# Performance work log

Measured on AMD Instinct MI355X. Metric: run time of the kernel, lower is better.

Reference implementation:

```python
import jax, jax.numpy as jnp
import numpy as np

N_EXPERTS = 8
TOP_K = 2


def setup_inputs() -> dict:
    key = jax.random.key(0)
    ks = jax.random.split(key, 5)
    B, T, D, E, H = 4, 2048, 1024, N_EXPERTS, 2730  # H = int(2*D*4/3)
    x = jax.random.normal(ks[0], (B, T, D), dtype=jnp.float32)
    gate_w = jax.random.normal(ks[1], (E, D), dtype=jnp.float32) * 0.02
    w1 = jax.random.normal(ks[2], (E, H, D), dtype=jnp.float32) * 0.02
    w3 = jax.random.normal(ks[3], (E, H, D), dtype=jnp.float32) * 0.02
    w2 = jax.random.normal(ks[4], (E, D, H), dtype=jnp.float32) * 0.02
    return {"x": x, "gate_w": gate_w, "w1": w1, "w3": w3, "w2": w2}


def reference(x, gate_w, w1, w3, w2):
    B, T, D = x.shape
    E = gate_w.shape[0]
    x_flat = x.reshape(-1, D)  # [N, D], N = B*T
    N = x_flat.shape[0]

    # Router: top-k over softmax probabilities, renormalized over selected experts
    logits = x_flat @ gate_w.T                      # [N, E]
    probs = jax.nn.softmax(logits, axis=-1)         # [N, E]
    top_v, top_i = jax.lax.top_k(probs, TOP_K)      # [N, K]
    top_v = top_v / jnp.sum(top_v, axis=-1, keepdims=True)

    # Dense combine weights [N, E]: weight of expert e for each token (0 if not selected).
    # top_k indices are distinct per token, so scatter-add equals scatter-set here.
    combine = jnp.zeros((N, E), dtype=x.dtype).at[
        jnp.arange(N)[:, None], top_i
    ].add(top_v)

    # Weighted combine of SwiGLU experts (loop over small fixed expert count).
    out = jnp.zeros_like(x_flat)
    for e in range(E):
        gate = jax.nn.silu(x_flat @ w1[e].T)        # [N, H]
        up = x_flat @ w3[e].T                       # [N, H]
        y = (gate * up) @ w2[e].T                   # [N, D]
        out = out + combine[:, e:e + 1] * y

    aux_loss = jnp.asarray(0.0, dtype=x.dtype)  # use_aux_loss=False / eval mode
    return out.reshape(B, T, D), aux_loss
```

## Files before the change

### kernel.cpp

```cpp
#include <hip/hip_runtime.h>
#include <hip/hip_bf16.h>

#define N_TOK 8192
#define D_DIM 1024
#define E_NUM 8
#define H_DIM 2730
#define HP    2816
#define NP    5632
#define NROWS (N_TOK*2)
#define MAXTILES 136
#define MAXT256  72

typedef __bf16 bf16;
typedef __bf16 bf16x8 __attribute__((ext_vector_type(8)));
typedef __bf16 bf16x4 __attribute__((ext_vector_type(4)));
typedef float  f32x4  __attribute__((ext_vector_type(4)));

__device__ __forceinline__ void gload_lds16(const bf16* g, bf16* l) {
  __builtin_amdgcn_global_load_lds((const __attribute__((address_space(1))) void*)g,
                                   (__attribute__((address_space(3))) void*)l, 16, 0, 0);
}
#define VMCNT(n) asm volatile("s_waitcnt vmcnt(" #n ")" ::: "memory")
#define BAR() __builtin_amdgcn_s_barrier()

__global__ void conv13_kernel(const float* __restrict__ w1, const float* __restrict__ w3,
                              bf16* __restrict__ Bp) {
  int i = blockIdx.x * blockDim.x + threadIdx.x;
  if (i >= E_NUM * NP * 128) return;
  int c8 = i & 127;
  int r  = (i >> 7) % NP;
  int e  = i / (NP * 128);
  int hc = ((r >> 5) << 4) + (r & 15);
  bf16x8 o;
  if (hc < H_DIM) {
    const float* s = (((r >> 4) & 1) ? w3 : w1) + ((long)e * H_DIM + hc) * D_DIM + c8 * 8;
    float4 a0 = ((const float4*)s)[0], a1 = ((const float4*)s)[1];
    o[0]=(bf16)a0.x; o[1]=(bf16)a0.y; o[2]=(bf16)a0.z; o[3]=(bf16)a0.w;
    o[4]=(bf16)a1.x; o[5]=(bf16)a1.y; o[6]=(bf16)a1.z; o[7]=(bf16)a1.w;
  } else {
    #pragma unroll
    for (int j = 0; j < 8; j++) o[j] = (bf16)0.f;
  }
  ((bf16x8*)Bp)[i] = o;
}

__global__ void conv_w2_kernel(const float* __restrict__ src, bf16* __restrict__ dst) {
  int i = blockIdx.x * blockDim.x + threadIdx.x;
  if (i >= E_NUM * D_DIM * (HP / 8)) return;
  int c8 = i % (HP / 8);
  int row = i / (HP / 8);
  int c = c8 * 8;
  const float* s = src + (long)row * H_DIM + c;
  bf16x8 o;
  #pragma unroll
  for (int j = 0; j < 8; j++) o[j] = (c + j < H_DIM) ? (bf16)s[j] : (bf16)0.f;
  ((bf16x8*)dst)[i] = o;
}

__global__ void router_kernel(const float* __restrict__ x, const float* __restrict__ gw,
                              int* __restrict__ topi, float* __restrict__ topw,
                              int* __restrict__ counts) {
  int t = blockIdx.x * (blockDim.x >> 6) + (threadIdx.x >> 6);
  int lane = threadIdx.x & 63;
  if (t >= N_TOK) return;
  const float* xr = x + (long)t * D_DIM;
  float acc[E_NUM];
  #pragma unroll
  for (int e = 0; e < E_NUM; e++) acc[e] = 0.f;
  for (int j = 0; j < D_DIM / 64; j++) {
    float xv = xr[j * 64 + lane];
    #pragma unroll
    for (int e = 0; e < E_NUM; e++) acc[e] += xv * gw[e * D_DIM + j * 64 + lane];
  }
  #pragma unroll
  for (int e = 0; e < E_NUM; e++) {
    float v = acc[e];
    #pragma unroll
    for (int s = 32; s > 0; s >>= 1) v += __shfl_xor(v, s, 64);
    acc[e] = v;
  }
  if (lane == 0) {
    int b0 = -1, b1 = -1; float v0 = -1e30f, v1 = -1e30f;
    #pragma unroll
    for (int e = 0; e < E_NUM; e++) {
      float v = acc[e];
      if (v > v0) { v1 = v0; b1 = b0; v0 = v; b0 = e; }
      else if (v > v1) { v1 = v; b1 = e; }
    }
    float w0 = 1.f / (1.f + expf(v1 - v0));
    topi[t * 2] = b0; topi[t * 2 + 1] = b1;
    topw[t * 2] = w0; topw[t * 2 + 1] = 1.f - w0;
    atomicAdd(&counts[b0], 1); atomicAdd(&counts[b1], 1);
  }
}

__global__ void tiles_kernel(const int* __restrict__ counts, int* __restrict__ offs,
                             int* __restrict__ tlist, int* __restrict__ tlist2) {
  if (threadIdx.x == 0) {
    int s = 0, idx = 0, idx2 = 0;
    for (int e = 0; e < E_NUM; e++) {
      offs[e] = s;
      int ne = counts[e];
      s += ne;
      int nt = (ne + 127) >> 7;
      for (int t = 0; t < nt; t++) tlist[idx++] = (e << 8) | t;
      int nt2 = (ne + 255) >> 8;
      for (int t = 0; t < nt2; t++) tlist2[idx2++] = (e << 8) | t;
    }
    offs[E_NUM] = s;
    for (; idx < MAXTILES; idx++) tlist[idx] = -1;
    for (; idx2 < MAXT256; idx2++) tlist2[idx2] = -1;
  }
}

__global__ void scatter_kernel(const int* __restrict__ topi, const float* __restrict__ topw,
                               const int* __restrict__ offs, int* __restrict__ cursor,
                               int* __restrict__ rowmap, float* __restrict__ roww,
                               int* __restrict__ rowoftok) {
  int i = blockIdx.x * blockDim.x + threadIdx.x;
  if (i >= NROWS) return;
  int e = topi[i];
  int pos = atomicAdd(&cursor[e], 1);
  int row = offs[e] + pos;
  rowmap[row] = i >> 1;
  roww[row] = topw[i];
  rowoftok[i] = row;
}

__global__ void gather_kernel(const float* __restrict__ x, const int* __restrict__ rowmap,
                              bf16* __restrict__ Xg) {
  int r = blockIdx.x * (blockDim.x >> 6) + (threadIdx.x >> 6);
  int lane = threadIdx.x & 63;
  if (r >= NROWS) return;
  int t = rowmap[r];
  const float4* src = (const float4*)(x + (long)t * D_DIM);
  bf16x4* dst = (bf16x4*)(Xg + (long)r * D_DIM);
  #pragma unroll
  for (int j = 0; j < 4; j++) {
    float4 v = src[j * 64 + lane];
    bf16x4 o; o[0]=(bf16)v.x; o[1]=(bf16)v.y; o[2]=(bf16)v.z; o[3]=(bf16)v.w;
    dst[j * 64 + lane] = o;
  }
}

__global__ void combine_kernel(const bf16* __restrict__ y, const int* __restrict__ rowoftok,
                               const float* __restrict__ topw, float* __restrict__ out) {
  int t = blockIdx.x * (blockDim.x >> 6) + (threadIdx.x >> 6);
  int lane = threadIdx.x & 63;
  if (t >= N_TOK) return;
  int r0 = rowoftok[t * 2], r1 = rowoftok[t * 2 + 1];
  float w0 = topw[t * 2], w1 = topw[t * 2 + 1];
  const bf16x8* y0 = (const bf16x8*)(y + (long)r0 * D_DIM);
  const bf16x8* y1 = (const bf16x8*)(y + (long)r1 * D_DIM);
  float* o = out + (long)t * D_DIM;
  #pragma unroll
  for (int j = 0; j < 2; j++) {
    bf16x8 a = y0[j * 64 + lane], b = y1[j * 64 + lane];
    float4 v0, v1;
    v0.x = w0*(float)a[0] + w1*(float)b[0]; v0.y = w0*(float)a[1] + w1*(float)b[1];
    v0.z = w0*(float)a[2] + w1*(float)b[2]; v0.w = w0*(float)a[3] + w1*(float)b[3];
    v1.x = w0*(float)a[4] + w1*(float)b[4]; v1.y = w0*(float)a[5] + w1*(float)b[5];
    v1.z = w0*(float)a[6] + w1*(float)b[6]; v1.w = w0*(float)a[7] + w1*(float)b[7];
    float4* op = (float4*)(o + (j * 64 + lane) * 8);
    op[0] = v0; op[1] = v1;
  }
}

#define G1_READ_A(MH, OB) do { \
    _Pragma("unroll") for (int m_ = 0; m_ < 4; m_++) \
    _Pragma("unroll") for (int ks_ = 0; ks_ < 2; ks_++) \
      aF[m_][ks_] = *(const bf16x8*)&smem[(OB) + ((MH)*128 + wr*64 + m_*16 + fr)*64 + ((ks_*4 + hi) ^ fr7)*8]; \
  } while (0)
#define G1_READ_B(NH, OB) do { \
    _Pragma("unroll") for (int n_ = 0; n_ < 2; n_++) \
    _Pragma("unroll") for (int ks_ = 0; ks_ < 2; ks_++) \
      bF[n_][ks_] = *(const bf16x8*)&smem[(OB) + 16384 + ((NH)*128 + wc*32 + n_*16 + fr)*64 + ((ks_*4 + hi) ^ fr7)*8]; \
  } while (0)
#define G1_MFMA(MH, NH) do { \
    __builtin_amdgcn_s_setprio(1); \
    _Pragma("unroll") for (int m_ = 0; m_ < 4; m_++) \
    _Pragma("unroll") for (int n_ = 0; n_ < 2; n_++) \
    _Pragma("unroll") for (int ks_ = 0; ks_ < 2; ks_++) \
      acc[MH][NH][m_][n_] = __builtin_amdgcn_mfma_f32_16x16x32_bf16(aF[m_][ks_], bF[n_][ks_], acc[MH][NH][m_][n_], 0, 0, 0); \
    __builtin_amdgcn_s_setprio(0); \
  } while (0)
#define G1_STAGE_A(NB, HM, KT) do { \
    _Pragma("unroll") for (int L_ = 0; L_ < 2; L_++) \
      gload_lds16(aP[HM][L_] + (KT)*64, smem + (NB)*32768 + ((HM)*128 + wv*16 + L_*8)*64); \
  } while (0)
#define G1_STAGE_B(NB, HM, KT) do { \
    _Pragma("unroll") for (int L_ = 0; L_ < 2; L_++) \
      gload_lds16(bP[HM][L_] + (KT)*64, smem + (NB)*32768 + 16384 + ((HM)*128 + wv*16 + L_*8)*64); \
  } while (0)

__global__ __launch_bounds__(512, 2) void gemm1_kernel(
    const bf16* __restrict__ Xg, const bf16* __restrict__ Bp,
    const int* __restrict__ counts, const int* __restrict__ offs,
    const int* __restrict__ tlist2, bf16* __restrict__ h) {
  int te = tlist2[blockIdx.x];
  if (te < 0) return;
  int e = te >> 8, tm = te & 255;
  int ne = counts[e];
  int row_base = offs[e];
  int n0 = blockIdx.y * 256;

  __shared__ bf16 smem[2 * 32768];
  int tid = threadIdx.x, wv = tid >> 6, lane = tid & 63;
  int wr = wv >> 2, wc = wv & 3;
  int fr = lane & 15, hi = lane >> 4, fr7 = lane & 7;
  int l8 = lane >> 3;
  int sx = ((lane & 7) ^ (l8 & 7)) * 8;

  f32x4 acc[2][2][4][2];
  #pragma unroll
  for (int a = 0; a < 2; a++)
    #pragma unroll
    for (int b = 0; b < 2; b++)
      #pragma unroll
      for (int m = 0; m < 4; m++)
        #pragma unroll
        for (int n = 0; n < 2; n++) acc[a][b][m][n] = (f32x4)0.f;

  const bf16* Bpe = Bp + (long)e * NP * D_DIM;
  const bf16* aP[2][2];
  const bf16* bP[2][2];
  #pragma unroll
  for (int hm = 0; hm < 2; hm++)
    #pragma unroll
    for (int L = 0; L < 2; L++) {
      int rt = tm * 256 + hm * 128 + wv * 16 + L * 8 + l8;
      aP[hm][L] = Xg + (long)(row_base + min(rt, ne - 1)) * D_DIM + sx;
      int rb = n0 + hm * 128 + wv * 16 + L * 8 + l8;
      bP[hm][L] = Bpe + (long)rb * D_DIM + sx;
    }

  bf16x8 aF[4][2], bF[2][2];

  G1_STAGE_B(0, 0, 0); G1_STAGE_A(0, 0, 0); G1_STAGE_A(0, 1, 0); G1_STAGE_B(0, 1, 0);
  VMCNT(4); BAR();

  for (int t = 0; t < 15; t++) {
    int ob = (t & 1) << 15;
    int nb = (t + 1) & 1;
    G1_READ_A(0, ob); G1_READ_B(0, ob);
    G1_STAGE_B(nb, 0, t + 1);
    VMCNT(4); BAR(); G1_MFMA(0, 0); BAR();
    G1_READ_A(1, ob);
    G1_STAGE_A(nb, 0, t + 1);
    VMCNT(4); BAR(); G1_MFMA(1, 0); BAR();
    G1_READ_B(1, ob);
    G1_STAGE_A(nb, 1, t + 1);
    BAR(); G1_MFMA(1, 1); BAR();
    G1_READ_A(0, ob);
    G1_STAGE_B(nb, 1, t + 1);
    VMCNT(4); BAR(); G1_MFMA(0, 1); BAR();
  }
  {
    const int ob = 32768;
    G1_READ_A(0, ob); G1_READ_B(0, ob);
    VMCNT(2); BAR(); G1_MFMA(0, 0); BAR();
    G1_READ_A(1, ob);
    VMCNT(0); BAR(); G1_MFMA(1, 0); BAR();
    G1_READ_B(1, ob);
    BAR(); G1_MFMA(1, 1); BAR();
    G1_READ_A(0, ob);
    G1_MFMA(0, 1);
  }

  int crow4 = hi * 4, ccol = fr;
  #pragma unroll
  for (int mh = 0; mh < 2; mh++)
    #pragma unroll
    for (int m = 0; m < 4; m++)
      #pragma unroll
      for (int j = 0; j < 4; j++) {
        int rloc = tm * 256 + mh * 128 + wr * 64 + m * 16 + crow4 + j;
        if (rloc < ne) {
          long hrow = (long)(row_base + rloc) * HP;
          #pragma unroll
          for (int nh = 0; nh < 2; nh++) {
            int hc0 = (n0 + nh * 128 + wc * 32) >> 1;
            float g = acc[mh][nh][m][0][j], u = acc[mh][nh][m][1][j];
            h[hrow + hc0 + ccol] = (bf16)((g / (1.f + __expf(-g))) * u);
          }
        }
      }
}

#define G2_STAGE(OFF, K0) do { \
    _Pragma("unroll") for (int i_ = 0; i_ < 2; i_++) \
      gload_lds16(aptr[i_] + (K0), &smem2[(OFF) + (i_ * 4 + w) * 512]); \
    _Pragma("unroll") for (int j_ = 0; j_ < 4; j_++) \
      gload_lds16(bptr[j_] + (K0), &smem2[(OFF) + 4096 + (j_ * 4 + w) * 512]); \
  } while (0)
#define G2_COMPUTE(OFF) do { \
    bf16x8 af[4], bfr[8]; \
    _Pragma("unroll") for (int m_ = 0; m_ < 4; m_++) af[m_] = *(const bf16x8*)&smem2[(OFF) + (wr * 64 + m_ * 16 + fr) * 32 + qp]; \
    _Pragma("unroll") for (int n_ = 0; n_ < 8; n_++) bfr[n_] = *(const bf16x8*)&smem2[(OFF) + 4096 + (wc * 128 + n_ * 16 + fr) * 32 + qp]; \
    __builtin_amdgcn_s_setprio(1); \
    _Pragma("unroll") for (int m_ = 0; m_ < 4; m_++) \
    _Pragma("unroll") for (int n_ = 0; n_ < 8; n_++) \
      acc[m_][n_] = __builtin_amdgcn_mfma_f32_16x16x32_bf16(af[m_], bfr[n_], acc[m_][n_], 0, 0, 0); \
    __builtin_amdgcn_s_setprio(0); \
  } while (0)

__global__ __launch_bounds__(256, 2) void gemm2_kernel(
    const bf16* __restrict__ h, const bf16* __restrict__ w2b,
    const int* __restrict__ counts, const int* __restrict__ offs,
    const int* __restrict__ tlist, bf16* __restrict__ y) {
  int te = tlist[blockIdx.x];
  if (te < 0) return;
  int e = te >> 8, tm = te & 255;
  int ne = counts[e];
  int row_base = offs[e];
  int n0 = blockIdx.y * 256;

  __shared__ bf16 smem2[3 * 12288];
  int tid = threadIdx.x, w = tid >> 6, lane = tid & 63;
  int wr = w >> 1, wc = w & 1;
  int seg_c = (((lane & 3) ^ ((lane >> 3) & 3))) * 8;
  int fr = lane & 15;
  int qp = (((lane >> 4) ^ ((fr >> 1) & 3))) * 8;

  f32x4 acc[4][8];
  #pragma unroll
  for (int m = 0; m < 4; m++)
    #pragma unroll
    for (int n = 0; n < 8; n++) acc[m][n] = (f32x4)0.f;

  const bf16* w2e = w2b + (long)e * D_DIM * HP;
  const bf16* aptr[2];
  const bf16* bptr[4];
  #pragma unroll
  for (int i = 0; i < 2; i++) {
    int ra = row_base + min(tm * 128 + (i * 4 + w) * 16 + (lane >> 2), ne - 1);
    aptr[i] = h + (long)ra * HP + seg_c;
  }
  #pragma unroll
  for (int j = 0; j < 4; j++) {
    int rb = n0 + (j * 4 + w) * 16 + (lane >> 2);
    bptr[j] = w2e + (long)rb * HP + seg_c;
  }

  int o0 = 0, o1 = 12288, o2 = 24576;
  G2_STAGE(o0, 0);
  G2_STAGE(o1, 32);
  #define G2_ROT() do { int t_ = o0; o0 = o1; o1 = o2; o2 = t_; } while (0)
  for (int t = 0; t < HP / 32 - 2; t++) {
    G2_STAGE(o2, (t + 2) * 32);
    VMCNT(12);
    BAR();
    G2_COMPUTE(o0);
    BAR();
    G2_ROT();
  }
  VMCNT(6); BAR(); G2_COMPUTE(o0); BAR(); G2_ROT();
  VMCNT(0); BAR(); G2_COMPUTE(o0);

  int crow4 = (lane >> 4) * 4, ccol = lane & 15;
  #pragma unroll
  for (int m = 0; m < 4; m++)
    #pragma unroll
    for (int j = 0; j < 4; j++) {
      int rloc = tm * 128 + wr * 64 + m * 16 + crow4 + j;
      if (rloc < ne) {
        long yrow = (long)(row_base + rloc) * D_DIM;
        #pragma unroll
        for (int n = 0; n < 8; n++) {
          int col = n0 + wc * 128 + n * 16 + ccol;
          y[yrow + col] = (bf16)acc[m][n][j];
        }
      }
    }
}

extern "C" void kernel_launch(void* const* d_in, const int* in_sizes, int n_in,
                              void* d_out, int out_size, void* d_ws, size_t ws_size,
                              hipStream_t stream) {
  const float* x  = (const float*)d_in[0];
  const float* gw = (const float*)d_in[1];
  const float* w1 = (const float*)d_in[2];
  const float* w3 = (const float*)d_in[3];
  const float* w2 = (const float*)d_in[4];
  float* out = (float*)d_out;

  char* ws = (char*)d_ws;
  int*   counts   = (int*)(ws);
  int*   cursor   = (int*)(ws + 64);
  int*   offs     = (int*)(ws + 128);
  int*   tlist    = (int*)(ws + 192);
  int*   tlist2   = (int*)(ws + 768);
  int*   topi     = (int*)(ws + 2048);
  float* topw     = (float*)(ws + 2048 + 65536);
  int*   rowmap   = (int*)(ws + 2048 + 131072);
  float* roww     = (float*)(ws + 2048 + 196608);
  int*   rowoftok = (int*)(ws + 2048 + 262144);
  char*  big      = ws + 2048 + 327680;
  bf16* Bp   = (bf16*)big;
  bf16* w2b  = (bf16*)big;
  bf16* Xg   = Bp + (size_t)E_NUM * NP * D_DIM;
  bf16* hbuf = Xg + (size_t)NROWS * D_DIM;
  bf16* ybuf = Xg;

  hipMemsetAsync((char*)d_out + (size_t)(out_size - 1) * sizeof(float), 0, sizeof(float), stream);
  hipMemsetAsync(ws, 0, 256, stream);

  int nbp = E_NUM * NP * 128;
  conv13_kernel<<<(nbp + 255) / 256, 256, 0, stream>>>(w1, w3, Bp);

  router_kernel<<<N_TOK / 4, 256, 0, stream>>>(x, gw, topi, topw, counts);
  tiles_kernel<<<1, 64, 0, stream>>>(counts, offs, tlist, tlist2);
  scatter_kernel<<<(NROWS + 255) / 256, 256, 0, stream>>>(topi, topw, offs, cursor, rowmap, roww, rowoftok);
  gather_kernel<<<NROWS / 4, 256, 0, stream>>>(x, rowmap, Xg);

  dim3 g1(MAXT256, NP / 256);
  gemm1_kernel<<<g1, 512, 0, stream>>>(Xg, Bp, counts, offs, tlist2, hbuf);

  int w2n = E_NUM * D_DIM * (HP / 8);
  conv_w2_kernel<<<(w2n + 255) / 256, 256, 0, stream>>>(w2, w2b);

  dim3 g2(MAXTILES, 4);
  gemm2_kernel<<<g2, 256, 0, stream>>>(hbuf, w2b, counts, offs, tlist, ybuf);
  combine_kernel<<<N_TOK / 4, 256, 0, stream>>>(ybuf, rowoftok, topw, out);
}
```

Measured before the change: 752.6 us.

## Unify both expert GEMMs on a 256x256 tile with a four-stage K=32 pipeline

Both expert GEMMs now share one macro-based mainloop. It uses 256x256 output tiles with 512 threads, K steps of 32, and a four-deep global-to-LDS ring buffer, replacing gemm1's two-buffer K=64 schedule. gemm2 moves from 128x128-row tiles with 256 threads to the same 256-row tiles driven by tlist2, so the 128-row tile list is dropped. The aim is more operand reuse per tile and deeper latency hiding. In exchange, gemm2 has fewer blocks (72x4 grid) and more padded rows per expert, and gemm1 issues more barriers per unit of K.

```diff
diff --git a/kernel.cpp b/kernel.cpp
--- a/kernel.cpp
+++ b/kernel.cpp
@@ -8,7 +8,6 @@
 #define HP    2816
 #define NP    5632
 #define NROWS (N_TOK*2)
-#define MAXTILES 136
 #define MAXT256  72
 
 typedef __bf16 bf16;
@@ -95,20 +94,17 @@
 }
 
 __global__ void tiles_kernel(const int* __restrict__ counts, int* __restrict__ offs,
-                             int* __restrict__ tlist, int* __restrict__ tlist2) {
+                             int* __restrict__ tlist2) {
   if (threadIdx.x == 0) {
-    int s = 0, idx = 0, idx2 = 0;
+    int s = 0, idx2 = 0;
     for (int e = 0; e < E_NUM; e++) {
       offs[e] = s;
       int ne = counts[e];
       s += ne;
-      int nt = (ne + 127) >> 7;
-      for (int t = 0; t < nt; t++) tlist[idx++] = (e << 8) | t;
       int nt2 = (ne + 255) >> 8;
       for (int t = 0; t < nt2; t++) tlist2[idx2++] = (e << 8) | t;
     }
     offs[E_NUM] = s;
-    for (; idx < MAXTILES; idx++) tlist[idx] = -1;
     for (; idx2 < MAXT256; idx2++) tlist2[idx2] = -1;
   }
 }
@@ -166,32 +162,51 @@
   }
 }
 
-#define G1_READ_A(MH, OB) do { \
+
+#define STAGE4(T) do { int sb_ = ((T) & 3) * 8192; \
+    gload_lds16(aSrc0 + (T) * 32, smem + sb_ + wv * 512); \
+    gload_lds16(aSrc1 + (T) * 32, smem + sb_ + 4096 + wv * 512); \
+    gload_lds16(bSrc0 + (T) * 32, smem + 32768 + sb_ + wv * 512); \
+    gload_lds16(bSrc1 + (T) * 32, smem + 32768 + sb_ + 4096 + wv * 512); \
+  } while (0)
+
+#define PH0(SB) do { \
+    bf16x8 aF[4]; \
     _Pragma("unroll") for (int m_ = 0; m_ < 4; m_++) \
-    _Pragma("unroll") for (int ks_ = 0; ks_ < 2; ks_++) \
-      aF[m_][ks_] = *(const bf16x8*)&smem[(OB) + ((MH)*128 + wr*64 + m_*16 + fr)*64 + ((ks_*4 + hi) ^ fr7)*8]; \
-  } while (0)
-#define G1_READ_B(NH, OB) do { \
-    _Pragma("unroll") for (int n_ = 0; n_ < 2; n_++) \
-    _Pragma("unroll") for (int ks_ = 0; ks_ < 2; ks_++) \
-      bF[n_][ks_] = *(const bf16x8*)&smem[(OB) + 16384 + ((NH)*128 + wc*32 + n_*16 + fr)*64 + ((ks_*4 + hi) ^ fr7)*8]; \
-  } while (0)
-#define G1_MFMA(MH, NH) do { \
+      aF[m_] = *(const bf16x8*)&smem[(SB) + (wr * 64 + m_ * 16 + fr) * 32 + qp]; \
+    _Pragma("unroll") for (int q_ = 0; q_ < 4; q_++) \
+      bF[q_] = *(const bf16x8*)&smem[32768 + (SB) + ((q_ >> 1) * 128 + wc * 32 + (q_ & 1) * 16 + fr) * 32 + qp]; \
     __builtin_amdgcn_s_setprio(1); \
     _Pragma("unroll") for (int m_ = 0; m_ < 4; m_++) \
-    _Pragma("unroll") for (int n_ = 0; n_ < 2; n_++) \
-    _Pragma("unroll") for (int ks_ = 0; ks_ < 2; ks_++) \
-      acc[MH][NH][m_][n_] = __builtin_amdgcn_mfma_f32_16x16x32_bf16(aF[m_][ks_], bF[n_][ks_], acc[MH][NH][m_][n_], 0, 0, 0); \
+    _Pragma("unroll") for (int q_ = 0; q_ < 4; q_++) \
+      acc[0][q_ >> 1][m_][q_ & 1] = __builtin_amdgcn_mfma_f32_16x16x32_bf16(aF[m_], bF[q_], acc[0][q_ >> 1][m_][q_ & 1], 0, 0, 0); \
     __builtin_amdgcn_s_setprio(0); \
   } while (0)
-#define G1_STAGE_A(NB, HM, KT) do { \
-    _Pragma("unroll") for (int L_ = 0; L_ < 2; L_++) \
-      gload_lds16(aP[HM][L_] + (KT)*64, smem + (NB)*32768 + ((HM)*128 + wv*16 + L_*8)*64); \
+
+#define PH1(SB) do { \
+    bf16x8 aF[4]; \
+    _Pragma("unroll") for (int m_ = 0; m_ < 4; m_++) \
+      aF[m_] = *(const bf16x8*)&smem[(SB) + (128 + wr * 64 + m_ * 16 + fr) * 32 + qp]; \
+    __builtin_amdgcn_s_setprio(1); \
+    _Pragma("unroll") for (int m_ = 0; m_ < 4; m_++) \
+    _Pragma("unroll") for (int q_ = 0; q_ < 4; q_++) \
+      acc[1][q_ >> 1][m_][q_ & 1] = __builtin_amdgcn_mfma_f32_16x16x32_bf16(aF[m_], bF[q_], acc[1][q_ >> 1][m_][q_ & 1], 0, 0, 0); \
+    __builtin_amdgcn_s_setprio(0); \
   } while (0)
-#define G1_STAGE_B(NB, HM, KT) do { \
-    _Pragma("unroll") for (int L_ = 0; L_ < 2; L_++) \
-      gload_lds16(bP[HM][L_] + (KT)*64, smem + (NB)*32768 + 16384 + ((HM)*128 + wv*16 + L_*8)*64); \
-  } while (0)
+
+#define GEMM_PREAMBLE() \
+  int tid = threadIdx.x, wv = tid >> 6, lane = tid & 63; \
+  int wr = wv >> 2, wc = wv & 3; \
+  int fr = lane & 15, hi = lane >> 4; \
+  int qp = (hi ^ ((fr >> 1) & 3)) * 8; \
+  int srcq = ((lane & 3) ^ ((lane >> 3) & 3)) * 8; \
+  int srow = lane >> 2; \
+  f32x4 acc[2][2][4][2]; \
+  _Pragma("unroll") for (int a = 0; a < 2; a++) \
+  _Pragma("unroll") for (int b = 0; b < 2; b++) \
+  _Pragma("unroll") for (int m = 0; m < 4; m++) \
+  _Pragma("unroll") for (int n = 0; n < 2; n++) acc[a][b][m][n] = (f32x4)0.f; \
+  bf16x8 bF[4];
 
 __global__ __launch_bounds__(512, 2) void gemm1_kernel(
     const bf16* __restrict__ Xg, const bf16* __restrict__ Bp,
@@ -204,70 +219,30 @@
   int row_base = offs[e];
   int n0 = blockIdx.y * 256;
 
-  __shared__ bf16 smem[2 * 32768];
-  int tid = threadIdx.x, wv = tid >> 6, lane = tid & 63;
-  int wr = wv >> 2, wc = wv & 3;
-  int fr = lane & 15, hi = lane >> 4, fr7 = lane & 7;
-  int l8 = lane >> 3;
-  int sx = ((lane & 7) ^ (l8 & 7)) * 8;
-
-  f32x4 acc[2][2][4][2];
-  #pragma unroll
-  for (int a = 0; a < 2; a++)
-    #pragma unroll
-    for (int b = 0; b < 2; b++)
-      #pragma unroll
-      for (int m = 0; m < 4; m++)
-        #pragma unroll
-        for (int n = 0; n < 2; n++) acc[a][b][m][n] = (f32x4)0.f;
+  __shared__ bf16 smem[65536];
+  GEMM_PREAMBLE();
 
   const bf16* Bpe = Bp + (long)e * NP * D_DIM;
-  const bf16* aP[2][2];
-  const bf16* bP[2][2];
-  #pragma unroll
-  for (int hm = 0; hm < 2; hm++)
-    #pragma unroll
-    for (int L = 0; L < 2; L++) {
-      int rt = tm * 256 + hm * 128 + wv * 16 + L * 8 + l8;
-      aP[hm][L] = Xg + (long)(row_base + min(rt, ne - 1)) * D_DIM + sx;
-      int rb = n0 + hm * 128 + wv * 16 + L * 8 + l8;
-      bP[hm][L] = Bpe + (long)rb * D_DIM + sx;
-    }
-
-  bf16x8 aF[4][2], bF[2][2];
-
-  G1_STAGE_B(0, 0, 0); G1_STAGE_A(0, 0, 0); G1_STAGE_A(0, 1, 0); G1_STAGE_B(0, 1, 0);
-  VMCNT(4); BAR();
-
-  for (int t = 0; t < 15; t++) {
-    int ob = (t & 1) << 15;
-    int nb = (t + 1) & 1;
-    G1_READ_A(0, ob); G1_READ_B(0, ob);
-    G1_STAGE_B(nb, 0, t + 1);
-    VMCNT(4); BAR(); G1_MFMA(0, 0); BAR();
-    G1_READ_A(1, ob);
-    G1_STAGE_A(nb, 0, t + 1);
-    VMCNT(4); BAR(); G1_MFMA(1, 0); BAR();
-    G1_READ_B(1, ob);
-    G1_STAGE_A(nb, 1, t + 1);
-    BAR(); G1_MFMA(1, 1); BAR();
-    G1_READ_A(0, ob);
-    G1_STAGE_B(nb, 1, t + 1);
-    VMCNT(4); BAR(); G1_MFMA(0, 1); BAR();
-  }
-  {
-    const int ob = 32768;
-    G1_READ_A(0, ob); G1_READ_B(0, ob);
-    VMCNT(2); BAR(); G1_MFMA(0, 0); BAR();
-    G1_READ_A(1, ob);
-    VMCNT(0); BAR(); G1_MFMA(1, 0); BAR();
-    G1_READ_B(1, ob);
-    BAR(); G1_MFMA(1, 1); BAR();
-    G1_READ_A(0, ob);
-    G1_MFMA(0, 1);
-  }
-
-  int crow4 = hi * 4, ccol = fr;
+  int ra0 = row_base + min(tm * 256 + wv * 16 + srow, ne - 1);
+  int ra1 = row_base + min(tm * 256 + 128 + wv * 16 + srow, ne - 1);
+  const bf16* aSrc0 = Xg + (long)ra0 * D_DIM + srcq;
+  const bf16* aSrc1 = Xg + (long)ra1 * D_DIM + srcq;
+  const bf16* bSrc0 = Bpe + (long)(n0 + wv * 16 + srow) * D_DIM + srcq;
+  const bf16* bSrc1 = Bpe + (long)(n0 + 128 + wv * 16 + srow) * D_DIM + srcq;
+
+  STAGE4(0); STAGE4(1); STAGE4(2);
+  for (int t = 0; t < 29; t++) {
+    STAGE4(t + 3);
+    VMCNT(12); BAR();
+    int sb = (t & 3) * 8192;
+    PH0(sb); BAR();
+    PH1(sb); BAR();
+  }
+  { VMCNT(8); BAR(); int sb = (29 & 3) * 8192; PH0(sb); BAR(); PH1(sb); BAR(); }
+  { VMCNT(4); BAR(); int sb = (30 & 3) * 8192; PH0(sb); BAR(); PH1(sb); BAR(); }
+  { VMCNT(0); BAR(); int sb = (31 & 3) * 8192; PH0(sb); BAR(); PH1(sb); }
+
+  int crow4 = hi * 4;
   #pragma unroll
   for (int mh = 0; mh < 2; mh++)
     #pragma unroll
@@ -281,97 +256,65 @@
           for (int nh = 0; nh < 2; nh++) {
             int hc0 = (n0 + nh * 128 + wc * 32) >> 1;
             float g = acc[mh][nh][m][0][j], u = acc[mh][nh][m][1][j];
-            h[hrow + hc0 + ccol] = (bf16)((g / (1.f + __expf(-g))) * u);
+            h[hrow + hc0 + fr] = (bf16)((g / (1.f + __expf(-g))) * u);
           }
         }
       }
 }
 
-#define G2_STAGE(OFF, K0) do { \
-    _Pragma("unroll") for (int i_ = 0; i_ < 2; i_++) \
-      gload_lds16(aptr[i_] + (K0), &smem2[(OFF) + (i_ * 4 + w) * 512]); \
-    _Pragma("unroll") for (int j_ = 0; j_ < 4; j_++) \
-      gload_lds16(bptr[j_] + (K0), &smem2[(OFF) + 4096 + (j_ * 4 + w) * 512]); \
-  } while (0)
-#define G2_COMPUTE(OFF) do { \
-    bf16x8 af[4], bfr[8]; \
-    _Pragma("unroll") for (int m_ = 0; m_ < 4; m_++) af[m_] = *(const bf16x8*)&smem2[(OFF) + (wr * 64 + m_ * 16 + fr) * 32 + qp]; \
-    _Pragma("unroll") for (int n_ = 0; n_ < 8; n_++) bfr[n_] = *(const bf16x8*)&smem2[(OFF) + 4096 + (wc * 128 + n_ * 16 + fr) * 32 + qp]; \
-    __builtin_amdgcn_s_setprio(1); \
-    _Pragma("unroll") for (int m_ = 0; m_ < 4; m_++) \
-    _Pragma("unroll") for (int n_ = 0; n_ < 8; n_++) \
-      acc[m_][n_] = __builtin_amdgcn_mfma_f32_16x16x32_bf16(af[m_], bfr[n_], acc[m_][n_], 0, 0, 0); \
-    __builtin_amdgcn_s_setprio(0); \
-  } while (0)
-
-__global__ __launch_bounds__(256, 2) void gemm2_kernel(
+__global__ __launch_bounds__(512, 2) void gemm2_kernel(
     const bf16* __restrict__ h, const bf16* __restrict__ w2b,
     const int* __restrict__ counts, const int* __restrict__ offs,
-    const int* __restrict__ tlist, bf16* __restrict__ y) {
-  int te = tlist[blockIdx.x];
+    const int* __restrict__ tlist2, bf16* __restrict__ y) {
+  int te = tlist2[blockIdx.x];
   if (te < 0) return;
   int e = te >> 8, tm = te & 255;
   int ne = counts[e];
   int row_base = offs[e];
   int n0 = blockIdx.y * 256;
 
-  __shared__ bf16 smem2[3 * 12288];
-  int tid = threadIdx.x, w = tid >> 6, lane = tid & 63;
-  int wr = w >> 1, wc = w & 1;
-  int seg_c = (((lane & 3) ^ ((lane >> 3) & 3))) * 8;
-  int fr = lane & 15;
-  int qp = (((lane >> 4) ^ ((fr >> 1) & 3))) * 8;
-
-  f32x4 acc[4][8];
-  #pragma unroll
-  for (int m = 0; m < 4; m++)
-    #pragma unroll
-    for (int n = 0; n < 8; n++) acc[m][n] = (f32x4)0.f;
+  __shared__ bf16 smem[65536];
+  GEMM_PREAMBLE();
 
   const bf16* w2e = w2b + (long)e * D_DIM * HP;
-  const bf16* aptr[2];
-  const bf16* bptr[4];
-  #pragma unroll
-  for (int i = 0; i < 2; i++) {
-    int ra = row_base + min(tm * 128 + (i * 4 + w) * 16 + (lane >> 2), ne - 1);
-    aptr[i] = h + (long)ra * HP + seg_c;
-  }
-  #pragma unroll
-  for (int j = 0; j < 4; j++) {
-    int rb = n0 + (j * 4 + w) * 16 + (lane >> 2);
-    bptr[j] = w2e + (long)rb * HP + seg_c;
-  }
-
-  int o0 = 0, o1 = 12288, o2 = 24576;
-  G2_STAGE(o0, 0);
-  G2_STAGE(o1, 32);
-  #define G2_ROT() do { int t_ = o0; o0 = o1; o1 = o2; o2 = t_; } while (0)
-  for (int t = 0; t < HP / 32 - 2; t++) {
-    G2_STAGE(o2, (t + 2) * 32);
-    VMCNT(12);
-    BAR();
-    G2_COMPUTE(o0);
-    BAR();
-    G2_ROT();
-  }
-  VMCNT(6); BAR(); G2_COMPUTE(o0); BAR(); G2_ROT();
-  VMCNT(0); BAR(); G2_COMPUTE(o0);
-
-  int crow4 = (lane >> 4) * 4, ccol = lane & 15;
-  #pragma unroll
-  for (int m = 0; m < 4; m++)
-    #pragma unroll
-    for (int j = 0; j < 4; j++) {
-      int rloc = tm * 128 + wr * 64 + m * 16 + crow4 + j;
-      if (rloc < ne) {
-        long yrow = (long)(row_base + rloc) * D_DIM;
-        #pragma unroll
-        for (int n = 0; n < 8; n++) {
-          int col = n0 + wc * 128 + n * 16 + ccol;
-          y[yrow + col] = (bf16)acc[m][n][j];
+  int ra0 = row_base + min(tm * 256 + wv * 16 + srow, ne - 1);
+  int ra1 = row_base + min(tm * 256 + 128 + wv * 16 + srow, ne - 1);
+  const bf16* aSrc0 = h + (long)ra0 * HP + srcq;
+  const bf16* aSrc1 = h + (long)ra1 * HP + srcq;
+  const bf16* bSrc0 = w2e + (long)(n0 + wv * 16 + srow) * HP + srcq;
+  const bf16* bSrc1 = w2e + (long)(n0 + 128 + wv * 16 + srow) * HP + srcq;
+
+  STAGE4(0); STAGE4(1); STAGE4(2);
+  for (int t = 0; t < 85; t++) {
+    STAGE4(t + 3);
+    VMCNT(12); BAR();
+    int sb = (t & 3) * 8192;
+    PH0(sb); BAR();
+    PH1(sb); BAR();
+  }
+  { VMCNT(8); BAR(); int sb = (85 & 3) * 8192; PH0(sb); BAR(); PH1(sb); BAR(); }
+  { VMCNT(4); BAR(); int sb = (86 & 3) * 8192; PH0(sb); BAR(); PH1(sb); BAR(); }
+  { VMCNT(0); BAR(); int sb = (87 & 3) * 8192; PH0(sb); BAR(); PH1(sb); }
+
+  int crow4 = hi * 4;
+  #pragma unroll
+  for (int mh = 0; mh < 2; mh++)
+    #pragma unroll
+    for (int m = 0; m < 4; m++)
+      #pragma unroll
+      for (int j = 0; j < 4; j++) {
+        int rloc = tm * 256 + mh * 128 + wr * 64 + m * 16 + crow4 + j;
+        if (rloc < ne) {
+          long yrow = (long)(row_base + rloc) * D_DIM;
+          #pragma unroll
+          for (int nh = 0; nh < 2; nh++)
+            #pragma unroll
+            for (int n = 0; n < 2; n++) {
+              int col = n0 + nh * 128 + wc * 32 + n * 16 + fr;
+              y[yrow + col] = (bf16)acc[mh][nh][m][n][j];
+            }
         }
       }
-    }
 }
 
 extern "C" void kernel_launch(void* const* d_in, const int* in_sizes, int n_in,
@@ -388,7 +331,6 @@
   int*   counts   = (int*)(ws);
   int*   cursor   = (int*)(ws + 64);
   int*   offs     = (int*)(ws + 128);
-  int*   tlist    = (int*)(ws + 192);
   int*   tlist2   = (int*)(ws + 768);
   int*   topi     = (int*)(ws + 2048);
   float* topw     = (float*)(ws + 2048 + 65536);
@@ -409,7 +351,7 @@
   conv13_kernel<<<(nbp + 255) / 256, 256, 0, stream>>>(w1, w3, Bp);
 
   router_kernel<<<N_TOK / 4, 256, 0, stream>>>(x, gw, topi, topw, counts);
-  tiles_kernel<<<1, 64, 0, stream>>>(counts, offs, tlist, tlist2);
+  tiles_kernel<<<1, 64, 0, stream>>>(counts, offs, tlist2);
   scatter_kernel<<<(NROWS + 255) / 256, 256, 0, stream>>>(topi, topw, offs, cursor, rowmap, roww, rowoftok);
   gather_kernel<<<NROWS / 4, 256, 0, stream>>>(x, rowmap, Xg);
 
@@ -419,7 +361,7 @@
   int w2n = E_NUM * D_DIM * (HP / 8);
   conv_w2_kernel<<<(w2n + 255) / 256, 256, 0, stream>>>(w2, w2b);
 
-  dim3 g2(MAXTILES, 4);
-  gemm2_kernel<<<g2, 256, 0, stream>>>(hbuf, w2b, counts, offs, tlist, ybuf);
+  dim3 g2(MAXT256, D_DIM / 256);
+  gemm2_kernel<<<g2, 512, 0, stream>>>(hbuf, w2b, counts, offs, tlist2, ybuf);
   combine_kernel<<<N_TOK / 4, 256, 0, stream>>>(ybuf, rowoftok, topw, out);
 }
```

Result: slower. 795.4 us (+5.7%).
